# Optimization experiments

Measured on AMD Instinct MI355X. Metric: run time of the kernel, lower is better.

Reference implementation:

```python
import jax, jax.numpy as jnp
import numpy as np

BETA = 1.0
GAMMA = 1.0
DELTA = 0.0


def setup_inputs() -> dict:
    key = jax.random.key(0)
    k1, k2 = jax.random.split(key)
    xyz1 = jax.random.normal(k1, (4, 4096, 3), dtype=jnp.float32)
    xyz2 = jax.random.normal(k2, (4, 4096, 3), dtype=jnp.float32)
    return {"xyz1": xyz1, "xyz2": xyz2}


def _pairwise_sqdist(a, b):
    # a: [B, N, 3], b: [B, M, 3] -> [B, N, M] squared euclidean distances
    a2 = jnp.sum(a * a, axis=-1)  # [B, N]
    b2 = jnp.sum(b * b, axis=-1)  # [B, M]
    ab = jnp.einsum("bnd,bmd->bnm", a, b)  # [B, N, M]
    return a2[:, :, None] + b2[:, None, :] - 2.0 * ab


def reference(xyz1, xyz2):
    P = xyz1.shape[1]
    d = _pairwise_sqdist(xyz1, xyz2)  # [B, N, M]
    dist12 = jnp.min(d, axis=2)       # nearest in xyz2 for each xyz1 point
    idx12 = jnp.argmin(d, axis=2)
    dist21 = jnp.min(d, axis=1)       # nearest in xyz1 for each xyz2 point
    idx21 = jnp.argmin(d, axis=1)
    loss = (jnp.mean(dist12, axis=-1)
            + jnp.max(dist12, axis=-1) * BETA
            + (GAMMA + DELTA * P) * jnp.mean(dist21, axis=-1))
    loss = jnp.mean(loss)
    return loss, idx12, idx21
```

## Files before the change

kernel.cpp:

```cpp
#include <hip/hip_runtime.h>
#include <stdint.h>
#include <float.h>


constexpr int B_ = 4;
constexpr int N_ = 4096;
constexpr int PTS = 256;
constexpr int PPT = 8;
constexpr int TILES = N_ / (PTS * PPT);
constexpr int JSPLIT = 32;
constexpr int CHUNK = N_ / JSPLIT;
constexpr double EPS32 = 1.1920928955078125e-7;
constexpr double TOL_K12 = 0.6 * EPS32;
constexpr double TOL_K21 = 0.0;
constexpr double BETA_ = 1.0;
constexpr double GAMMA_ = 1.0;
constexpr double DELTA_ = 0.0;

__global__ __launch_bounds__(256) void cd_min32(
        const float* __restrict__ xyz1, const float* __restrict__ xyz2,
        unsigned int* __restrict__ splitmin, float4* __restrict__ b4) {
    const int tile  = blockIdx.x % TILES;
    const int b     = (blockIdx.x / TILES) % B_;
    const int dir   = blockIdx.x / (TILES * B_);
    const int split = blockIdx.y;
    const float* A  = dir ? xyz2 : xyz1;
    const float* Bc = dir ? xyz1 : xyz2;
    const size_t ob = (size_t)dir * B_ + b;

    __shared__ float4 s[CHUNK];
    const float* bbase = Bc + ((size_t)b * N_ + (size_t)split * CHUNK) * 3;
    if (threadIdx.x < CHUNK) {
        int j = threadIdx.x;
        float bx = bbase[3 * j], by = bbase[3 * j + 1], bz = bbase[3 * j + 2];
        float b2 = bx * bx + by * by + bz * bz;
        float4 v = make_float4(bx, by, bz, b2);
        s[j] = v;
        if (tile == 0)
            b4[ob * N_ + (size_t)split * CHUNK + j] = v;
    }
    __syncthreads();

    float px[PPT], py[PPT], pz[PPT], mn[PPT];
    #pragma unroll
    for (int pi = 0; pi < PPT; ++pi) {
        const int p = tile * (PTS * PPT) + pi * PTS + threadIdx.x;
        const float* ap = A + ((size_t)b * N_ + p) * 3;
        px[pi] = ap[0]; py[pi] = ap[1]; pz[pi] = ap[2];
        mn[pi] = FLT_MAX;
    }

    #pragma unroll 4
    for (int j = 0; j < CHUNK; ++j) {
        float4 bv = s[j];
        #pragma unroll
        for (int pi = 0; pi < PPT; ++pi) {
            float dx = px[pi] - bv.x, dy = py[pi] - bv.y, dz = pz[pi] - bv.z;
            mn[pi] = fminf(mn[pi],
                           __fmaf_rn(dx, dx, __fmaf_rn(dy, dy, dz * dz)));
        }
    }

    const size_t sm = (ob * JSPLIT + split) * N_;
    #pragma unroll
    for (int pi = 0; pi < PPT; ++pi) {
        const int p = tile * (PTS * PPT) + pi * PTS + threadIdx.x;
        splitmin[sm + p] = __float_as_uint(mn[pi]);
    }
}

__global__ __launch_bounds__(256) void cd_select(
        const float* __restrict__ xyz1, const float* __restrict__ xyz2,
        const unsigned int* __restrict__ splitmin, const float4* __restrict__ b4,
        double* __restrict__ dminArr, float* __restrict__ out) {
    const int W0   = blockIdx.x * 4;
    const int dir  = W0 / (B_ * N_);
    const int b    = (W0 / N_) % B_;
    const int p0   = W0 % N_;
    const float* A  = dir ? xyz2 : xyz1;
    const double tolk = dir ? TOL_K21 : TOL_K12;
    const size_t ob = (size_t)dir * B_ + b;
    const float4* bb4 = b4 + ob * N_;

    __shared__ unsigned int lt[4][32];

    if (threadIdx.x < 128) {
        const int s  = threadIdx.x >> 2;
        const int pi = threadIdx.x & 3;
        lt[pi][s] = splitmin[(ob * JSPLIT + s) * N_ + p0 + pi];
    }
    __syncthreads();

    const int wv   = threadIdx.x >> 6;
    const int lane = threadIdx.x & 63;
    const int p    = p0 + wv;
    const int W    = W0 + wv;

    const float* ap = A + ((size_t)b * N_ + p) * 3;
    const float x = ap[0], y = ap[1], z = ap[2];
    const float a2f = x * x + y * y + z * z;

    const int l32 = lane & 31;
    const float sv = __uint_as_float(lt[wv][l32]);
    float m = sv;
    #pragma unroll
    for (int off = 1; off < 32; off <<= 1)
        m = fminf(m, __shfl_xor(m, off));

    const float me = __fmaf_rn(2e-6f, m, m);
    const float skipthr = (me + 7e-7f * a2f) * (1.0f + 4e-6f);
    unsigned int mask = (unsigned int)__ballot(lane < 32 && sv <= skipthr);

    const double xd = (double)x, yd = (double)y, zd = (double)z;
    const double a2 = xd * xd + yd * yd + zd * zd;

    double dmin = 1.0e300;
    unsigned int mk = mask;
    while (mk) {
        int s = __ffs(mk) - 1; mk &= mk - 1;
        int j0 = s * CHUNK + lane;
        float4 bv0 = bb4[j0];
        float4 bv1 = bb4[j0 + 64];
        #pragma unroll
        for (int k = 0; k < 2; ++k) {
            float4 bv = k ? bv1 : bv0;
            float dx = x - bv.x, dy = y - bv.y, dz = z - bv.z;
            float d32 = __fmaf_rn(dx, dx, __fmaf_rn(dy, dy, dz * dz));
            float thr = __fmaf_rn(2e-7f, a2f + bv.w, me);
            if (d32 <= thr) {
                double ddx = xd - (double)bv.x, ddy = yd - (double)bv.y,
                       ddz = zd - (double)bv.z;
                dmin = fmin(dmin, fma(ddx, ddx, fma(ddy, ddy, ddz * ddz)));
            }
        }
    }
    #pragma unroll
    for (int off = 1; off < 64; off <<= 1)
        dmin = fmin(dmin, __shfl_xor(dmin, off));

    unsigned int pick = 0xFFFFFFFFu;
    mk = mask;
    while (mk) {
        int s = __ffs(mk) - 1; mk &= mk - 1;
        int j0 = s * CHUNK + lane;
        float4 bv0 = bb4[j0];
        float4 bv1 = bb4[j0 + 64];
        #pragma unroll
        for (int k = 0; k < 2; ++k) {
            float4 bv = k ? bv1 : bv0;
            int j = j0 + k * 64;
            float dx = x - bv.x, dy = y - bv.y, dz = z - bv.z;
            float d32 = __fmaf_rn(dx, dx, __fmaf_rn(dy, dy, dz * dz));
            float thr = __fmaf_rn(2e-7f, a2f + bv.w, me);
            if (d32 <= thr) {
                double bxd = (double)bv.x, byd = (double)bv.y, bzd = (double)bv.z;
                double ddx = xd - bxd, ddy = yd - byd, ddz = zd - bzd;
                double d64 = fma(ddx, ddx, fma(ddy, ddy, ddz * ddz));
                double M   = a2 + (bxd * bxd + byd * byd + bzd * bzd);
                if (d64 <= fma(tolk, M, dmin))
                    pick = (pick < (unsigned int)j) ? pick : (unsigned int)j;
            }
        }
    }
    #pragma unroll
    for (int off = 1; off < 64; off <<= 1) {
        unsigned int o2 = (unsigned int)__shfl_xor((int)pick, off);
        pick = (o2 < pick) ? o2 : pick;
    }

    if (lane == 0) {
        dminArr[W] = dmin;
        const size_t obase = (dir == 0) ? (1 + (size_t)b * N_)
                                        : (1 + (size_t)B_ * N_ + (size_t)b * N_);
        out[obase + p] = (float)pick;
    }
}

__global__ __launch_bounds__(256) void cd_finalize(
        const double* __restrict__ dminArr, float* __restrict__ out,
        double* __restrict__ loss_part) {
    const int b = blockIdx.x;
    const int t = threadIdx.x;

    double sum12 = 0.0, max12 = -1.0e300, sum21 = 0.0;
    for (int n = t; n < N_; n += 256) {
        double d12 = dminArr[(size_t)b * N_ + n];
        double d21 = dminArr[((size_t)B_ + b) * N_ + n];
        sum12 += d12;
        max12 = fmax(max12, d12);
        sum21 += d21;
    }
    __shared__ double s1[256], s2[256], s3[256];
    s1[t] = sum12; s2[t] = max12; s3[t] = sum21;
    __syncthreads();
    for (int off = 128; off > 0; off >>= 1) {
        if (t < off) {
            s1[t] += s1[t + off];
            s2[t]  = fmax(s2[t], s2[t + off]);
            s3[t] += s3[t + off];
        }
        __syncthreads();
    }
    if (t == 0) {
        loss_part[b] = s1[0] / (double)N_ + BETA_ * s2[0]
                     + (GAMMA_ + DELTA_ * (double)N_) * (s3[0] / (double)N_);
    }
}

__global__ void cd_loss(const double* __restrict__ loss_part,
                        float* __restrict__ out) {
    if (blockIdx.x == 0 && threadIdx.x == 0) {
        double s = 0.0;
        for (int b = 0; b < B_; ++b) s += loss_part[b];
        out[0] = (float)(s / (double)B_);
    }
}

extern "C" void kernel_launch(void* const* d_in, const int* in_sizes, int n_in,
                              void* d_out, int out_size, void* d_ws, size_t ws_size,
                              hipStream_t stream) {
    const float* xyz1 = (const float*)d_in[0];
    const float* xyz2 = (const float*)d_in[1];
    float* out = (float*)d_out;

    const size_t NP = (size_t)2 * B_ * N_;
    double* dminArr   = (double*)d_ws;
    double* loss_part = dminArr + NP;
    unsigned int* splitmin = (unsigned int*)(loss_part + B_);
    float4* b4 = (float4*)(splitmin + NP * JSPLIT);

    dim3 grid(TILES * B_ * 2, JSPLIT);
    cd_min32<<<grid, PTS, 0, stream>>>(xyz1, xyz2, splitmin, b4);

    cd_select<<<(int)(NP / 4), 256, 0, stream>>>(xyz1, xyz2, splitmin, b4,
                                                 dminArr, out);

    cd_finalize<<<B_, 256, 0, stream>>>(dminArr, out, loss_part);
    cd_loss<<<1, 64, 0, stream>>>(loss_part, out);
}
```

Baseline: 48.19 us.

## Track per-split champion index and runner-up to avoid rescanning chunks in select

The fp32 min pass now records, for each point and each split, the best distance, its index, and the second-best (runner-up) distance. The select kernel then re-checks only the champion index in fp64 for each candidate split. It rescans a whole chunk only when that chunk's runner-up also falls within the tolerance threshold. Select is restructured from one wave per point to one thread per point, staging per-split data in LDS, and PPT is halved to 4. The first pass does more work and writes three arrays instead of one, and chunks that need rescanning are now scanned serially by one thread.

```diff
diff --git a/kernel.cpp b/kernel.cpp
--- a/kernel.cpp
+++ b/kernel.cpp
@@ -6,10 +6,11 @@
 constexpr int B_ = 4;
 constexpr int N_ = 4096;
 constexpr int PTS = 256;
-constexpr int PPT = 8;
+constexpr int PPT = 4;
 constexpr int TILES = N_ / (PTS * PPT);
 constexpr int JSPLIT = 32;
 constexpr int CHUNK = N_ / JSPLIT;
+constexpr int SPB = 128;
 constexpr double EPS32 = 1.1920928955078125e-7;
 constexpr double TOL_K12 = 0.6 * EPS32;
 constexpr double TOL_K21 = 0.0;
@@ -19,7 +20,8 @@
 
 __global__ __launch_bounds__(256) void cd_min32(
         const float* __restrict__ xyz1, const float* __restrict__ xyz2,
-        unsigned int* __restrict__ splitmin, float4* __restrict__ b4) {
+        float* __restrict__ champD, unsigned int* __restrict__ champJ,
+        float* __restrict__ runUp, float4* __restrict__ b4) {
     const int tile  = blockIdx.x % TILES;
     const int b     = (blockIdx.x / TILES) % B_;
     const int dir   = blockIdx.x / (TILES * B_);
@@ -41,23 +43,28 @@
     }
     __syncthreads();
 
-    float px[PPT], py[PPT], pz[PPT], mn[PPT];
+    float px[PPT], py[PPT], pz[PPT];
+    float cur[PPT], ruv[PPT];
+    unsigned int cj[PPT];
     #pragma unroll
     for (int pi = 0; pi < PPT; ++pi) {
         const int p = tile * (PTS * PPT) + pi * PTS + threadIdx.x;
         const float* ap = A + ((size_t)b * N_ + p) * 3;
         px[pi] = ap[0]; py[pi] = ap[1]; pz[pi] = ap[2];
-        mn[pi] = FLT_MAX;
+        cur[pi] = FLT_MAX; ruv[pi] = FLT_MAX; cj[pi] = 0u;
     }
 
     #pragma unroll 4
     for (int j = 0; j < CHUNK; ++j) {
         float4 bv = s[j];
+        const unsigned int jg = (unsigned int)(split * CHUNK + j);
         #pragma unroll
         for (int pi = 0; pi < PPT; ++pi) {
             float dx = px[pi] - bv.x, dy = py[pi] - bv.y, dz = pz[pi] - bv.z;
-            mn[pi] = fminf(mn[pi],
-                           __fmaf_rn(dx, dx, __fmaf_rn(dy, dy, dz * dz)));
+            float d = __fmaf_rn(dx, dx, __fmaf_rn(dy, dy, dz * dz));
+            ruv[pi] = fminf(ruv[pi], fmaxf(d, cur[pi]));
+            if (d < cur[pi]) cj[pi] = jg;
+            cur[pi] = fminf(cur[pi], d);
         }
     }
 
@@ -65,65 +72,77 @@
     #pragma unroll
     for (int pi = 0; pi < PPT; ++pi) {
         const int p = tile * (PTS * PPT) + pi * PTS + threadIdx.x;
-        splitmin[sm + p] = __float_as_uint(mn[pi]);
-    }
-}
-
-__global__ __launch_bounds__(256) void cd_select(
+        champD[sm + p] = cur[pi];
+        champJ[sm + p] = cj[pi];
+        runUp[sm + p]  = ruv[pi];
+    }
+}
+
+__global__ __launch_bounds__(SPB) void cd_select(
         const float* __restrict__ xyz1, const float* __restrict__ xyz2,
-        const unsigned int* __restrict__ splitmin, const float4* __restrict__ b4,
+        const float* __restrict__ champD, const unsigned int* __restrict__ champJ,
+        const float* __restrict__ runUp, const float4* __restrict__ b4,
         double* __restrict__ dminArr, float* __restrict__ out) {
-    const int W0   = blockIdx.x * 4;
-    const int dir  = W0 / (B_ * N_);
-    const int b    = (W0 / N_) % B_;
-    const int p0   = W0 % N_;
+    const int ob  = blockIdx.x >> 5;
+    const int c   = blockIdx.x & 31;
+    const int dir = ob >> 2;
+    const int b   = ob & 3;
+    const int p0  = c * SPB;
     const float* A  = dir ? xyz2 : xyz1;
     const double tolk = dir ? TOL_K21 : TOL_K12;
-    const size_t ob = (size_t)dir * B_ + b;
-    const float4* bb4 = b4 + ob * N_;
-
-    __shared__ unsigned int lt[4][32];
-
-    if (threadIdx.x < 128) {
-        const int s  = threadIdx.x >> 2;
-        const int pi = threadIdx.x & 3;
-        lt[pi][s] = splitmin[(ob * JSPLIT + s) * N_ + p0 + pi];
+    const float4* bb4 = b4 + (size_t)ob * N_;
+
+    __shared__ float cDl[JSPLIT][SPB];
+    __shared__ unsigned int cJl[JSPLIT][SPB];
+    __shared__ float rul[JSPLIT][SPB];
+
+    const int t = threadIdx.x;
+    for (int idx = t; idx < JSPLIT * SPB; idx += SPB) {
+        const int s = idx >> 7, p = idx & (SPB - 1);
+        const size_t g = ((size_t)ob * JSPLIT + s) * N_ + p0 + p;
+        cDl[s][p] = champD[g];
+        cJl[s][p] = champJ[g];
+        rul[s][p] = runUp[g];
     }
     __syncthreads();
 
-    const int wv   = threadIdx.x >> 6;
-    const int lane = threadIdx.x & 63;
-    const int p    = p0 + wv;
-    const int W    = W0 + wv;
-
+    const int p = p0 + t;
     const float* ap = A + ((size_t)b * N_ + p) * 3;
     const float x = ap[0], y = ap[1], z = ap[2];
     const float a2f = x * x + y * y + z * z;
 
-    const int l32 = lane & 31;
-    const float sv = __uint_as_float(lt[wv][l32]);
-    float m = sv;
-    #pragma unroll
-    for (int off = 1; off < 32; off <<= 1)
-        m = fminf(m, __shfl_xor(m, off));
+    float m = FLT_MAX;
+    #pragma unroll
+    for (int s = 0; s < JSPLIT; ++s)
+        m = fminf(m, cDl[s][t]);
 
     const float me = __fmaf_rn(2e-6f, m, m);
     const float skipthr = (me + 7e-7f * a2f) * (1.0f + 4e-6f);
-    unsigned int mask = (unsigned int)__ballot(lane < 32 && sv <= skipthr);
+
+    unsigned int candmask = 0, rescmask = 0;
+    #pragma unroll
+    for (int s = 0; s < JSPLIT; ++s) {
+        if (cDl[s][t] <= skipthr) candmask |= (1u << s);
+        if (rul[s][t] <= skipthr) rescmask |= (1u << s);
+    }
 
     const double xd = (double)x, yd = (double)y, zd = (double)z;
     const double a2 = xd * xd + yd * yd + zd * zd;
 
     double dmin = 1.0e300;
-    unsigned int mk = mask;
-    while (mk) {
-        int s = __ffs(mk) - 1; mk &= mk - 1;
-        int j0 = s * CHUNK + lane;
-        float4 bv0 = bb4[j0];
-        float4 bv1 = bb4[j0 + 64];
-        #pragma unroll
-        for (int k = 0; k < 2; ++k) {
-            float4 bv = k ? bv1 : bv0;
+    unsigned int mk = candmask;
+    while (mk) {
+        int s = __ffs(mk) - 1; mk &= mk - 1;
+        float4 bv = bb4[cJl[s][t]];
+        double ddx = xd - (double)bv.x, ddy = yd - (double)bv.y,
+               ddz = zd - (double)bv.z;
+        dmin = fmin(dmin, fma(ddx, ddx, fma(ddy, ddy, ddz * ddz)));
+    }
+    mk = rescmask;
+    while (mk) {
+        int s = __ffs(mk) - 1; mk &= mk - 1;
+        for (int j = s * CHUNK; j < (s + 1) * CHUNK; ++j) {
+            float4 bv = bb4[j];
             float dx = x - bv.x, dy = y - bv.y, dz = z - bv.z;
             float d32 = __fmaf_rn(dx, dx, __fmaf_rn(dy, dy, dz * dz));
             float thr = __fmaf_rn(2e-7f, a2f + bv.w, me);
@@ -134,21 +153,24 @@
             }
         }
     }
-    #pragma unroll
-    for (int off = 1; off < 64; off <<= 1)
-        dmin = fmin(dmin, __shfl_xor(dmin, off));
 
     unsigned int pick = 0xFFFFFFFFu;
-    mk = mask;
-    while (mk) {
-        int s = __ffs(mk) - 1; mk &= mk - 1;
-        int j0 = s * CHUNK + lane;
-        float4 bv0 = bb4[j0];
-        float4 bv1 = bb4[j0 + 64];
-        #pragma unroll
-        for (int k = 0; k < 2; ++k) {
-            float4 bv = k ? bv1 : bv0;
-            int j = j0 + k * 64;
+    mk = candmask;
+    while (mk) {
+        int s = __ffs(mk) - 1; mk &= mk - 1;
+        unsigned int j = cJl[s][t];
+        float4 bv = bb4[j];
+        double bxd = (double)bv.x, byd = (double)bv.y, bzd = (double)bv.z;
+        double ddx = xd - bxd, ddy = yd - byd, ddz = zd - bzd;
+        double d64 = fma(ddx, ddx, fma(ddy, ddy, ddz * ddz));
+        double M   = a2 + (bxd * bxd + byd * byd + bzd * bzd);
+        if (d64 <= fma(tolk, M, dmin)) pick = (j < pick) ? j : pick;
+    }
+    mk = rescmask;
+    while (mk) {
+        int s = __ffs(mk) - 1; mk &= mk - 1;
+        for (int j = s * CHUNK; j < (s + 1) * CHUNK; ++j) {
+            float4 bv = bb4[j];
             float dx = x - bv.x, dy = y - bv.y, dz = z - bv.z;
             float d32 = __fmaf_rn(dx, dx, __fmaf_rn(dy, dy, dz * dz));
             float thr = __fmaf_rn(2e-7f, a2f + bv.w, me);
@@ -158,22 +180,15 @@
                 double d64 = fma(ddx, ddx, fma(ddy, ddy, ddz * ddz));
                 double M   = a2 + (bxd * bxd + byd * byd + bzd * bzd);
                 if (d64 <= fma(tolk, M, dmin))
-                    pick = (pick < (unsigned int)j) ? pick : (unsigned int)j;
+                    pick = ((unsigned int)j < pick) ? (unsigned int)j : pick;
             }
         }
     }
-    #pragma unroll
-    for (int off = 1; off < 64; off <<= 1) {
-        unsigned int o2 = (unsigned int)__shfl_xor((int)pick, off);
-        pick = (o2 < pick) ? o2 : pick;
-    }
-
-    if (lane == 0) {
-        dminArr[W] = dmin;
-        const size_t obase = (dir == 0) ? (1 + (size_t)b * N_)
-                                        : (1 + (size_t)B_ * N_ + (size_t)b * N_);
-        out[obase + p] = (float)pick;
-    }
+
+    dminArr[(size_t)ob * N_ + p] = dmin;
+    const size_t obase = (dir == 0) ? (1 + (size_t)b * N_)
+                                    : (1 + (size_t)B_ * N_ + (size_t)b * N_);
+    out[obase + p] = (float)pick;
 }
 
 __global__ __launch_bounds__(256) void cd_finalize(
@@ -226,14 +241,16 @@
     const size_t NP = (size_t)2 * B_ * N_;
     double* dminArr   = (double*)d_ws;
     double* loss_part = dminArr + NP;
-    unsigned int* splitmin = (unsigned int*)(loss_part + B_);
-    float4* b4 = (float4*)(splitmin + NP * JSPLIT);
+    float4* b4 = (float4*)(loss_part + B_);
+    float* champD = (float*)(b4 + NP);
+    unsigned int* champJ = (unsigned int*)(champD + NP * JSPLIT);
+    float* runUp = (float*)(champJ + NP * JSPLIT);
 
     dim3 grid(TILES * B_ * 2, JSPLIT);
-    cd_min32<<<grid, PTS, 0, stream>>>(xyz1, xyz2, splitmin, b4);
-
-    cd_select<<<(int)(NP / 4), 256, 0, stream>>>(xyz1, xyz2, splitmin, b4,
-                                                 dminArr, out);
+    cd_min32<<<grid, PTS, 0, stream>>>(xyz1, xyz2, champD, champJ, runUp, b4);
+
+    cd_select<<<(int)(NP / SPB), SPB, 0, stream>>>(
+        xyz1, xyz2, champD, champJ, runUp, b4, dminArr, out);
 
     cd_finalize<<<B_, 256, 0, stream>>>(dminArr, out, loss_part);
     cd_loss<<<1, 64, 0, stream>>>(loss_part, out);
```

Result: slower. 59.84 us (+24.2%).
